# Kernel tuning notes

Measured on AMD Instinct MI355X. Metric: run time of the kernel, lower is better.

## Reference

```python
import jax, jax.numpy as jnp
import numpy as np

B, T, D = 16, 4096, 256


def setup_inputs() -> dict:
    key = jax.random.key(0)
    ks = jax.random.split(key, 10)
    s = 1.0 / np.sqrt(D)  # torch nn.Linear default init range
    inp = {
        "x": jax.random.normal(ks[0], (B, T, D), jnp.float32),
        "hidden": jax.random.normal(ks[1], (B, D), jnp.float32),
    }
    names = ["W0", "b0", "W1", "b1", "W2", "b2", "W3", "b3"]
    for i, n in enumerate(names):
        shape = (D, D) if n.startswith("W") else (D,)
        inp[n] = jax.random.uniform(ks[2 + i], shape, jnp.float32, -s, s)
    return inp


def _gln(x, W0, b0, W1, b1, W2, b2, W3, b3):
    # Two gated-linear blocks; the final Linear(hyper[-1], hidden_size) in the
    # original module is never applied by calc_gln (index == len-1 is skipped).
    h = (x @ W0.T + b0) * jax.nn.sigmoid(x @ W1.T + b1)
    return (h @ W2.T + b2) * jax.nn.sigmoid(h @ W3.T + b3)


def reference(x, hidden, W0, b0, W1, b1, W2, b2, W3, b3):
    b = _gln(x, W0, b0, W1, b1, W2, b2, W3, b3)  # [B, T, D]
    bt = jnp.swapaxes(b, 0, 1)  # [T, B, D] for time-major scan
    init = jax.nn.relu(bt[0] + jnp.roll(hidden, 1, -1))

    def step(prev, b_t):
        out = jax.nn.relu(b_t + jnp.roll(prev, 1, -1))
        return out, out

    last, ys = jax.lax.scan(step, init, bt[1:])
    outputs = jnp.concatenate([init[None], ys], axis=0)  # [T, B, D]
    outputs = jnp.swapaxes(outputs, 0, 1)  # [B, T, D]; squeeze(2) is a no-op for D>1
    return outputs, last
```

## Files before the change

kernel.cpp:

```cpp
#include <hip/hip_runtime.h>
#include <hip/hip_bf16.h>
#include <cstdint>
#include <cstddef>

typedef __bf16 bf16x8 __attribute__((ext_vector_type(8)));
typedef float  f32x4  __attribute__((ext_vector_type(4)));

static constexpr int B  = 16;
static constexpr int T  = 4096;
static constexpr int D  = 256;
static constexpr int M  = B * T;
static constexpr int SEGS = 64;
static constexpr int SEGL = T / SEGS;

__global__ void cvt_w(const float* __restrict__ W0, const float* __restrict__ W1,
                      const float* __restrict__ W2, const float* __restrict__ W3,
                      __bf16* __restrict__ wp) {
    int i = blockIdx.x * blockDim.x + threadIdx.x;
    int s    = i >> 14;
    int r    = i & 16383;
    int ks   = r >> 11;
    int fg   = (r >> 6) & 31;
    int lane = r & 63;
    int kg = lane >> 4, rl = lane & 15;
    int w = fg >> 2, f = fg & 3;
    int q = f >> 1, gate = f & 1;
    int rc = w * 32 + 2 * rl + q;
    const float* src = (s == 0) ? (gate ? W1 : W0) : (gate ? W3 : W2);
    const float* p = src + (size_t)rc * 256 + ks * 32 + kg * 8;
    bf16x8 o;
#pragma unroll
    for (int j = 0; j < 8; ++j) o[j] = (__bf16)p[j];
    *reinterpret_cast<bf16x8*>(wp + (size_t)s * 131072 +
                               ((size_t)((ks * 32 + fg) * 64 + lane)) * 8) = o;
}

__launch_bounds__(512, 4)
__global__ void gln_fused(const float* __restrict__ x,
                          const __bf16* __restrict__ wp,
                          const float* __restrict__ b0, const float* __restrict__ b1,
                          const float* __restrict__ b2, const float* __restrict__ b3,
                          float* __restrict__ out) {
    __shared__ char xlds[32768];
    __shared__ char hlds[32768];

    const int tid  = threadIdx.x;
    const int lane = tid & 63;
    const int wid  = tid >> 6;
    const int rl   = lane & 15;
    const int kg   = lane >> 4;
    const int row0 = blockIdx.x * 64;

    {
        int r  = tid >> 3;
        int c0 = tid & 7;
        const float* xr = x + (size_t)(row0 + r) * 256;
        float4 xa[4][2];
#pragma unroll
        for (int ci = 0; ci < 4; ++ci) {
            const float4* p = reinterpret_cast<const float4*>(xr + (c0 + ci * 8) * 8);
            xa[ci][0] = p[0];
            xa[ci][1] = p[1];
        }
#pragma unroll
        for (int ci = 0; ci < 4; ++ci) {
            int ck = c0 + ci * 8;
            bf16x8 o = { (__bf16)xa[ci][0].x, (__bf16)xa[ci][0].y,
                         (__bf16)xa[ci][0].z, (__bf16)xa[ci][0].w,
                         (__bf16)xa[ci][1].x, (__bf16)xa[ci][1].y,
                         (__bf16)xa[ci][1].z, (__bf16)xa[ci][1].w };
            *reinterpret_cast<bf16x8*>(&xlds[r * 512 + ((ck ^ (r & 7)) * 16)]) = o;
        }
    }
    __syncthreads();

    f32x4 acc[4][4];

    auto run_stage = [&](const char* alds, const __bf16* wps) {
#pragma unroll
        for (int m = 0; m < 4; ++m)
#pragma unroll
            for (int f = 0; f < 4; ++f) acc[m][f] = (f32x4){0.f, 0.f, 0.f, 0.f};
#pragma unroll 2
        for (int ks = 0; ks < 8; ++ks) {
            bf16x8 bR[4], aR[4];
#pragma unroll
            for (int f = 0; f < 4; ++f)
                bR[f] = *reinterpret_cast<const bf16x8*>(
                    wps + ((size_t)((ks * 32 + (wid * 4 + f)) * 64 + lane)) * 8);
#pragma unroll
            for (int m = 0; m < 4; ++m) {
                int row = m * 16 + rl;
                int ck  = (ks * 4 + kg) ^ (rl & 7);
                aR[m] = *reinterpret_cast<const bf16x8*>(&alds[row * 512 + ck * 16]);
            }
#pragma unroll
            for (int m = 0; m < 4; ++m)
#pragma unroll
                for (int f = 0; f < 4; ++f)
                    acc[m][f] = __builtin_amdgcn_mfma_f32_16x16x32_bf16(
                        aR[m], bR[f], acc[m][f], 0, 0, 0);
        }
    };

    run_stage(xlds, wp);
    {
        int rc0 = wid * 32 + 2 * rl;
        float2 bb0 = *reinterpret_cast<const float2*>(b0 + rc0);
        float2 bb1 = *reinterpret_cast<const float2*>(b1 + rc0);
        int colb = rc0 * 2;
        int ckb  = colb >> 4;
        int off  = colb & 15;
#pragma unroll
        for (int m = 0; m < 4; ++m)
#pragma unroll
            for (int j = 0; j < 4; ++j) {
                int row = m * 16 + kg * 4 + j;
                float he = (acc[m][0][j] + bb0.x) *
                           (1.0f / (1.0f + __expf(-(acc[m][1][j] + bb1.x))));
                float ho = (acc[m][2][j] + bb0.y) *
                           (1.0f / (1.0f + __expf(-(acc[m][3][j] + bb1.y))));
                unsigned short ue = __builtin_bit_cast(unsigned short, (__bf16)he);
                unsigned short uo = __builtin_bit_cast(unsigned short, (__bf16)ho);
                unsigned int u = ((unsigned int)uo << 16) | (unsigned int)ue;
                *reinterpret_cast<unsigned int*>(
                    &hlds[row * 512 + ((ckb ^ (row & 7)) * 16) + off]) = u;
            }
    }
    __syncthreads();

    run_stage(hlds, wp + 131072);
    {
        int rc0 = wid * 32 + 2 * rl;
        float2 bb2 = *reinterpret_cast<const float2*>(b2 + rc0);
        float2 bb3 = *reinterpret_cast<const float2*>(b3 + rc0);
#pragma unroll
        for (int m = 0; m < 4; ++m)
#pragma unroll
            for (int j = 0; j < 4; ++j) {
                int row = m * 16 + kg * 4 + j;
                float he = (acc[m][0][j] + bb2.x) *
                           (1.0f / (1.0f + __expf(-(acc[m][1][j] + bb3.x))));
                float ho = (acc[m][2][j] + bb2.y) *
                           (1.0f / (1.0f + __expf(-(acc[m][3][j] + bb3.y))));
                float2 o; o.x = he; o.y = ho;
                *reinterpret_cast<float2*>(out + (size_t)(row0 + row) * 256 + rc0) = o;
            }
    }
}

__global__ void scan_seg(const float* __restrict__ bmat, float2* __restrict__ seg_am) {
    int tid   = blockIdx.x * blockDim.x + threadIdx.x;
    int c     = tid & 255;
    int rest  = tid >> 8;
    int batch = rest & 15;
    int seg   = rest >> 4;
    const float* base = bmat + (size_t)batch * T * D;
    float A = 0.f, Mx = -1e30f;
    int t0 = seg * SEGL;
#pragma unroll 8
    for (int i = 0; i < SEGL; ++i) {
        int t = t0 + i;
        float v = base[(size_t)t * 256 + ((c + t) & 255)];
        A += v;
        Mx = fmaxf(Mx + v, 0.f);
    }
    float2 o; o.x = A; o.y = Mx;
    seg_am[(size_t)(batch * SEGS + seg) * 256 + c] = o;
}

__global__ void scan_bound(const float2* __restrict__ seg_am,
                           const float* __restrict__ hidden,
                           float* __restrict__ seg_state) {
    int tid   = blockIdx.x * blockDim.x + threadIdx.x;
    int c     = tid & 255;
    int batch = tid >> 8;
    float s = hidden[batch * 256 + ((c + 255) & 255)];
    for (int seg = 0; seg < SEGS; ++seg) {
        seg_state[(size_t)(batch * SEGS + seg) * 256 + c] = s;
        float2 am = seg_am[(size_t)(batch * SEGS + seg) * 256 + c];
        s = fmaxf(s + am.x, am.y);
    }
}

__global__ void scan_apply(float* __restrict__ bio,
                           const float* __restrict__ seg_state,
                           float* __restrict__ last) {
    int tid   = blockIdx.x * blockDim.x + threadIdx.x;
    int c     = tid & 255;
    int rest  = tid >> 8;
    int batch = rest & 15;
    int seg   = rest >> 4;
    float s = seg_state[(size_t)(batch * SEGS + seg) * 256 + c];
    float* base = bio + (size_t)batch * T * D;
    int t0 = seg * SEGL;
#pragma unroll 8
    for (int i = 0; i < SEGL; ++i) {
        int t = t0 + i;
        size_t idx = (size_t)t * 256 + ((c + t) & 255);
        float v = base[idx];
        s = fmaxf(s + v, 0.f);
        base[idx] = s;
    }
    if (seg == SEGS - 1) last[batch * 256 + ((c + 255) & 255)] = s;
}

extern "C" void kernel_launch(void* const* d_in, const int* in_sizes, int n_in,
                              void* d_out, int out_size, void* d_ws, size_t ws_size,
                              hipStream_t stream) {
    const float* x      = (const float*)d_in[0];
    const float* hidden = (const float*)d_in[1];
    const float* W0 = (const float*)d_in[2];
    const float* b0 = (const float*)d_in[3];
    const float* W1 = (const float*)d_in[4];
    const float* b1 = (const float*)d_in[5];
    const float* W2 = (const float*)d_in[6];
    const float* b2 = (const float*)d_in[7];
    const float* W3 = (const float*)d_in[8];
    const float* b3 = (const float*)d_in[9];

    float* out  = (float*)d_out;
    float* last = out + (size_t)M * D;

    char* ws = (char*)d_ws;
    __bf16* wpb       = (__bf16*)ws;
    float2* seg_am    = (float2*)(ws + 524288);
    float*  seg_state = (float*)(ws + 524288 + 2097152);

    cvt_w<<<128, 256, 0, stream>>>(W0, W1, W2, W3, wpb);
    gln_fused<<<M / 64, 512, 0, stream>>>(x, wpb, b0, b1, b2, b3, out);

    scan_seg<<<(B * D * SEGS) / 256, 256, 0, stream>>>(out, seg_am);
    scan_bound<<<B * D / 256, 256, 0, stream>>>(seg_am, hidden, seg_state);
    scan_apply<<<(B * D * SEGS) / 256, 256, 0, stream>>>(out, seg_state, last);
}
```

Measured before the change: 97.29 us.

## Fuse segment scan reduction into GLN GEMM kernel epilogue via LDS tile

The per-segment scan reduction (sum and max-plus prefix) is moved into the GEMM kernel's epilogue. Each 64-row block stages its fp32 output tile in LDS (dynamic shared memory, 64KB) and 256 threads compute the segment summary from it. This drops the scan_seg kernel launch and its full re-read of the output from global memory. It also adds setprio around the MFMA loop, plus extra barriers and a serial 64-step loop on half the threads at the end of each block.

```diff
diff --git a/kernel.cpp b/kernel.cpp
--- a/kernel.cpp
+++ b/kernel.cpp
@@ -40,9 +40,12 @@
                           const __bf16* __restrict__ wp,
                           const float* __restrict__ b0, const float* __restrict__ b1,
                           const float* __restrict__ b2, const float* __restrict__ b3,
-                          float* __restrict__ out) {
-    __shared__ char xlds[32768];
-    __shared__ char hlds[32768];
+                          float* __restrict__ out,
+                          float2* __restrict__ seg_am) {
+    extern __shared__ char smem[];
+    char* xlds = smem;
+    char* hlds = smem + 32768;
+    float* ftile = reinterpret_cast<float*>(smem);
 
     const int tid  = threadIdx.x;
     const int lane = tid & 63;
@@ -94,12 +97,14 @@
                 int ck  = (ks * 4 + kg) ^ (rl & 7);
                 aR[m] = *reinterpret_cast<const bf16x8*>(&alds[row * 512 + ck * 16]);
             }
+            __builtin_amdgcn_s_setprio(1);
 #pragma unroll
             for (int m = 0; m < 4; ++m)
 #pragma unroll
                 for (int f = 0; f < 4; ++f)
                     acc[m][f] = __builtin_amdgcn_mfma_f32_16x16x32_bf16(
                         aR[m], bR[f], acc[m][f], 0, 0, 0);
+            __builtin_amdgcn_s_setprio(0);
         }
     };
 
@@ -130,6 +135,7 @@
     __syncthreads();
 
     run_stage(hlds, wp + 131072);
+    __syncthreads();
     {
         int rc0 = wid * 32 + 2 * rl;
         float2 bb2 = *reinterpret_cast<const float2*>(b2 + rc0);
@@ -145,28 +151,27 @@
                            (1.0f / (1.0f + __expf(-(acc[m][3][j] + bb3.y))));
                 float2 o; o.x = he; o.y = ho;
                 *reinterpret_cast<float2*>(out + (size_t)(row0 + row) * 256 + rc0) = o;
+                *reinterpret_cast<float2*>(ftile + row * 256 + rc0) = o;
             }
     }
-}
-
-__global__ void scan_seg(const float* __restrict__ bmat, float2* __restrict__ seg_am) {
-    int tid   = blockIdx.x * blockDim.x + threadIdx.x;
-    int c     = tid & 255;
-    int rest  = tid >> 8;
-    int batch = rest & 15;
-    int seg   = rest >> 4;
-    const float* base = bmat + (size_t)batch * T * D;
-    float A = 0.f, Mx = -1e30f;
-    int t0 = seg * SEGL;
+    __syncthreads();
+
+    if (tid < 256) {
+        int c     = tid;
+        int batch = row0 >> 12;
+        int t0    = row0 & 4095;
+        int seg   = t0 >> 6;
+        int cc    = (c + t0) & 255;
+        float A = 0.f, Mx = -1e30f;
 #pragma unroll 8
-    for (int i = 0; i < SEGL; ++i) {
-        int t = t0 + i;
-        float v = base[(size_t)t * 256 + ((c + t) & 255)];
-        A += v;
-        Mx = fmaxf(Mx + v, 0.f);
-    }
-    float2 o; o.x = A; o.y = Mx;
-    seg_am[(size_t)(batch * SEGS + seg) * 256 + c] = o;
+        for (int i = 0; i < SEGL; ++i) {
+            float v = ftile[i * 256 + ((cc + i) & 255)];
+            A += v;
+            Mx = fmaxf(Mx + v, 0.f);
+        }
+        float2 o; o.x = A; o.y = Mx;
+        seg_am[(size_t)(batch * SEGS + seg) * 256 + c] = o;
+    }
 }
 
 __global__ void scan_bound(const float2* __restrict__ seg_am,
@@ -227,10 +232,16 @@
     float2* seg_am    = (float2*)(ws + 524288);
     float*  seg_state = (float*)(ws + 524288 + 2097152);
 
+    static bool attr_done = false;
+    if (!attr_done) {
+        hipFuncSetAttribute(reinterpret_cast<const void*>(&gln_fused),
+                            hipFuncAttributeMaxDynamicSharedMemorySize, 65536);
+        attr_done = true;
+    }
+
     cvt_w<<<128, 256, 0, stream>>>(W0, W1, W2, W3, wpb);
-    gln_fused<<<M / 64, 512, 0, stream>>>(x, wpb, b0, b1, b2, b3, out);
-
-    scan_seg<<<(B * D * SEGS) / 256, 256, 0, stream>>>(out, seg_am);
+    gln_fused<<<M / 64, 512, 65536, stream>>>(x, wpb, b0, b1, b2, b3, out, seg_am);
+
     scan_bound<<<B * D / 256, 256, 0, stream>>>(seg_am, hidden, seg_state);
     scan_apply<<<(B * D * SEGS) / 256, 256, 0, stream>>>(out, seg_state, last);
 }
```

Result: faster. 93.63 us (-3.8%).

## Shrink GLN row tile to 32 with 16 waves and reuse one LDS buffer

Applied to the files above, without the earlier changes.

The fused GLN kernel now handles 32 rows per block with 1024 threads (16 waves split into 2 row groups × 8 column groups) instead of 64 rows with 8 waves. Each wave holds a single 16-row A fragment and 4 accumulators, not 4×4, which cuts register pressure. The x tile and the intermediate h tile share one 16 KB LDS buffer, with an added barrier before h overwrites it. In exchange, each block re-reads the full packed weights from global/L2 for half as many rows, doubling weight traffic per output row.

```diff
diff --git a/kernel.cpp b/kernel.cpp
--- a/kernel.cpp
+++ b/kernel.cpp
@@ -35,117 +35,99 @@
                                ((size_t)((ks * 32 + fg) * 64 + lane)) * 8) = o;
 }
 
-__launch_bounds__(512, 4)
+__launch_bounds__(1024, 8)
 __global__ void gln_fused(const float* __restrict__ x,
                           const __bf16* __restrict__ wp,
                           const float* __restrict__ b0, const float* __restrict__ b1,
                           const float* __restrict__ b2, const float* __restrict__ b3,
                           float* __restrict__ out) {
-    __shared__ char xlds[32768];
-    __shared__ char hlds[32768];
+    __shared__ char tile[16384];
 
     const int tid  = threadIdx.x;
     const int lane = tid & 63;
     const int wid  = tid >> 6;
     const int rl   = lane & 15;
     const int kg   = lane >> 4;
-    const int row0 = blockIdx.x * 64;
+    const int cw   = wid & 7;
+    const int rw   = wid >> 3;
+    const int row0 = blockIdx.x * 32;
+
+    const __bf16* wv0 = wp + ((size_t)(cw * 4) * 64 + lane) * 8;
+    const __bf16* wv1 = wv0 + 131072;
 
     {
-        int r  = tid >> 3;
-        int c0 = tid & 7;
-        const float* xr = x + (size_t)(row0 + r) * 256;
-        float4 xa[4][2];
-#pragma unroll
-        for (int ci = 0; ci < 4; ++ci) {
-            const float4* p = reinterpret_cast<const float4*>(xr + (c0 + ci * 8) * 8);
-            xa[ci][0] = p[0];
-            xa[ci][1] = p[1];
-        }
-#pragma unroll
-        for (int ci = 0; ci < 4; ++ci) {
-            int ck = c0 + ci * 8;
-            bf16x8 o = { (__bf16)xa[ci][0].x, (__bf16)xa[ci][0].y,
-                         (__bf16)xa[ci][0].z, (__bf16)xa[ci][0].w,
-                         (__bf16)xa[ci][1].x, (__bf16)xa[ci][1].y,
-                         (__bf16)xa[ci][1].z, (__bf16)xa[ci][1].w };
-            *reinterpret_cast<bf16x8*>(&xlds[r * 512 + ((ck ^ (r & 7)) * 16)]) = o;
-        }
+        int r  = tid >> 5;
+        int c0 = tid & 31;
+        const float4* p = reinterpret_cast<const float4*>(
+            x + (size_t)(row0 + r) * 256 + c0 * 8);
+        float4 v0 = p[0], v1 = p[1];
+        bf16x8 o = { (__bf16)v0.x, (__bf16)v0.y, (__bf16)v0.z, (__bf16)v0.w,
+                     (__bf16)v1.x, (__bf16)v1.y, (__bf16)v1.z, (__bf16)v1.w };
+        *reinterpret_cast<bf16x8*>(&tile[r * 512 + ((c0 ^ (r & 7)) * 16)]) = o;
     }
     __syncthreads();
 
-    f32x4 acc[4][4];
-
-    auto run_stage = [&](const char* alds, const __bf16* wps) {
-#pragma unroll
-        for (int m = 0; m < 4; ++m)
-#pragma unroll
-            for (int f = 0; f < 4; ++f) acc[m][f] = (f32x4){0.f, 0.f, 0.f, 0.f};
+    f32x4 acc[4];
+
+    auto run_stage = [&](const __bf16* wvb) {
+#pragma unroll
+        for (int f = 0; f < 4; ++f) acc[f] = (f32x4){0.f, 0.f, 0.f, 0.f};
+        const int arow = (rw * 16 + rl) * 512;
 #pragma unroll 2
         for (int ks = 0; ks < 8; ++ks) {
-            bf16x8 bR[4], aR[4];
+            bf16x8 bR[4];
 #pragma unroll
             for (int f = 0; f < 4; ++f)
-                bR[f] = *reinterpret_cast<const bf16x8*>(
-                    wps + ((size_t)((ks * 32 + (wid * 4 + f)) * 64 + lane)) * 8);
-#pragma unroll
-            for (int m = 0; m < 4; ++m) {
-                int row = m * 16 + rl;
-                int ck  = (ks * 4 + kg) ^ (rl & 7);
-                aR[m] = *reinterpret_cast<const bf16x8*>(&alds[row * 512 + ck * 16]);
-            }
-#pragma unroll
-            for (int m = 0; m < 4; ++m)
-#pragma unroll
-                for (int f = 0; f < 4; ++f)
-                    acc[m][f] = __builtin_amdgcn_mfma_f32_16x16x32_bf16(
-                        aR[m], bR[f], acc[m][f], 0, 0, 0);
+                bR[f] = *reinterpret_cast<const bf16x8*>(wvb + ks * 16384 + f * 512);
+            int ck = (ks * 4 + kg) ^ (rl & 7);
+            bf16x8 aR = *reinterpret_cast<const bf16x8*>(&tile[arow + ck * 16]);
+#pragma unroll
+            for (int f = 0; f < 4; ++f)
+                acc[f] = __builtin_amdgcn_mfma_f32_16x16x32_bf16(aR, bR[f], acc[f],
+                                                                 0, 0, 0);
         }
     };
 
-    run_stage(xlds, wp);
+    const int rc0 = cw * 32 + 2 * rl;
+
+    run_stage(wv0);
+    __syncthreads();
     {
-        int rc0 = wid * 32 + 2 * rl;
         float2 bb0 = *reinterpret_cast<const float2*>(b0 + rc0);
         float2 bb1 = *reinterpret_cast<const float2*>(b1 + rc0);
-        int colb = rc0 * 2;
-        int ckb  = colb >> 4;
-        int off  = colb & 15;
-#pragma unroll
-        for (int m = 0; m < 4; ++m)
-#pragma unroll
-            for (int j = 0; j < 4; ++j) {
-                int row = m * 16 + kg * 4 + j;
-                float he = (acc[m][0][j] + bb0.x) *
-                           (1.0f / (1.0f + __expf(-(acc[m][1][j] + bb1.x))));
-                float ho = (acc[m][2][j] + bb0.y) *
-                           (1.0f / (1.0f + __expf(-(acc[m][3][j] + bb1.y))));
-                unsigned short ue = __builtin_bit_cast(unsigned short, (__bf16)he);
-                unsigned short uo = __builtin_bit_cast(unsigned short, (__bf16)ho);
-                unsigned int u = ((unsigned int)uo << 16) | (unsigned int)ue;
-                *reinterpret_cast<unsigned int*>(
-                    &hlds[row * 512 + ((ckb ^ (row & 7)) * 16) + off]) = u;
-            }
+        int cb  = rc0 * 2;
+        int ck  = cb >> 4;
+        int off = cb & 15;
+#pragma unroll
+        for (int j = 0; j < 4; ++j) {
+            int row = rw * 16 + kg * 4 + j;
+            float he = (acc[0][j] + bb0.x) *
+                       (1.0f / (1.0f + __expf(-(acc[1][j] + bb1.x))));
+            float ho = (acc[2][j] + bb0.y) *
+                       (1.0f / (1.0f + __expf(-(acc[3][j] + bb1.y))));
+            unsigned short ue = __builtin_bit_cast(unsigned short, (__bf16)he);
+            unsigned short uo = __builtin_bit_cast(unsigned short, (__bf16)ho);
+            unsigned int u = ((unsigned int)uo << 16) | (unsigned int)ue;
+            *reinterpret_cast<unsigned int*>(
+                &tile[row * 512 + ((ck ^ (row & 7)) * 16) + off]) = u;
+        }
     }
     __syncthreads();
 
-    run_stage(hlds, wp + 131072);
+    run_stage(wv1);
     {
-        int rc0 = wid * 32 + 2 * rl;
         float2 bb2 = *reinterpret_cast<const float2*>(b2 + rc0);
         float2 bb3 = *reinterpret_cast<const float2*>(b3 + rc0);
 #pragma unroll
-        for (int m = 0; m < 4; ++m)
-#pragma unroll
-            for (int j = 0; j < 4; ++j) {
-                int row = m * 16 + kg * 4 + j;
-                float he = (acc[m][0][j] + bb2.x) *
-                           (1.0f / (1.0f + __expf(-(acc[m][1][j] + bb3.x))));
-                float ho = (acc[m][2][j] + bb2.y) *
-                           (1.0f / (1.0f + __expf(-(acc[m][3][j] + bb3.y))));
-                float2 o; o.x = he; o.y = ho;
-                *reinterpret_cast<float2*>(out + (size_t)(row0 + row) * 256 + rc0) = o;
-            }
+        for (int j = 0; j < 4; ++j) {
+            int row = rw * 16 + kg * 4 + j;
+            float he = (acc[0][j] + bb2.x) *
+                       (1.0f / (1.0f + __expf(-(acc[1][j] + bb3.x))));
+            float ho = (acc[2][j] + bb2.y) *
+                       (1.0f / (1.0f + __expf(-(acc[3][j] + bb3.y))));
+            float2 o; o.x = he; o.y = ho;
+            *reinterpret_cast<float2*>(out + (size_t)(row0 + row) * 256 + rc0) = o;
+        }
     }
 }
 
@@ -228,7 +210,7 @@
     float*  seg_state = (float*)(ws + 524288 + 2097152);
 
     cvt_w<<<128, 256, 0, stream>>>(W0, W1, W2, W3, wpb);
-    gln_fused<<<M / 64, 512, 0, stream>>>(x, wpb, b0, b1, b2, b3, out);
+    gln_fused<<<M / 32, 1024, 0, stream>>>(x, wpb, b0, b1, b2, b3, out);
 
     scan_seg<<<(B * D * SEGS) / 256, 256, 0, stream>>>(out, seg_am);
     scan_bound<<<B * D / 256, 256, 0, stream>>>(seg_am, hidden, seg_state);
```

Result: slower. 129.9 us (+33.5%).

## Double-buffer weight fragments, reuse one LDS tile, change swizzle pattern

Applied to the files above, without the earlier changes.

Weight fragments for the next k-step are now prefetched from global memory into registers while MFMAs run on the current step, and the k loop is fully unrolled. The x and h tiles share a single 32 KB LDS buffer, with an extra barrier before h overwrites x, which halves LDS use per block and may allow more resident blocks. The XOR swizzle now shifts the row bits by two, which changes the LDS bank-conflict pattern. The extra prefetch registers could raise register pressure against the launch bound.

```diff
diff --git a/kernel.cpp b/kernel.cpp
--- a/kernel.cpp
+++ b/kernel.cpp
@@ -41,8 +41,7 @@
                           const float* __restrict__ b0, const float* __restrict__ b1,
                           const float* __restrict__ b2, const float* __restrict__ b3,
                           float* __restrict__ out) {
-    __shared__ char xlds[32768];
-    __shared__ char hlds[32768];
+    __shared__ char tile[32768];
 
     const int tid  = threadIdx.x;
     const int lane = tid & 63;
@@ -51,6 +50,16 @@
     const int kg   = lane >> 4;
     const int row0 = blockIdx.x * 64;
 
+    const __bf16* wv0 = wp + ((size_t)(wid * 4) * 64 + lane) * 8;
+    const __bf16* wv1 = wv0 + 131072;
+
+    bf16x8 bbuf[2][4];
+    auto loadB = [&](int p, const __bf16* wvb, int ks) {
+#pragma unroll
+        for (int f = 0; f < 4; ++f)
+            bbuf[p][f] = *reinterpret_cast<const bf16x8*>(wvb + ks * 16384 + f * 512);
+    };
+
     {
         int r  = tid >> 3;
         int c0 = tid & 7;
@@ -65,52 +74,54 @@
 #pragma unroll
         for (int ci = 0; ci < 4; ++ci) {
             int ck = c0 + ci * 8;
+            int pc = ck ^ ((r & 7) << 2);
             bf16x8 o = { (__bf16)xa[ci][0].x, (__bf16)xa[ci][0].y,
                          (__bf16)xa[ci][0].z, (__bf16)xa[ci][0].w,
                          (__bf16)xa[ci][1].x, (__bf16)xa[ci][1].y,
                          (__bf16)xa[ci][1].z, (__bf16)xa[ci][1].w };
-            *reinterpret_cast<bf16x8*>(&xlds[r * 512 + ((ck ^ (r & 7)) * 16)]) = o;
+            *reinterpret_cast<bf16x8*>(&tile[r * 512 + pc * 16]) = o;
         }
     }
+    loadB(0, wv0, 0);
     __syncthreads();
 
     f32x4 acc[4][4];
 
-    auto run_stage = [&](const char* alds, const __bf16* wps) {
+    auto run_stage = [&](const __bf16* wvb) {
 #pragma unroll
         for (int m = 0; m < 4; ++m)
 #pragma unroll
             for (int f = 0; f < 4; ++f) acc[m][f] = (f32x4){0.f, 0.f, 0.f, 0.f};
-#pragma unroll 2
+#pragma unroll
         for (int ks = 0; ks < 8; ++ks) {
-            bf16x8 bR[4], aR[4];
-#pragma unroll
-            for (int f = 0; f < 4; ++f)
-                bR[f] = *reinterpret_cast<const bf16x8*>(
-                    wps + ((size_t)((ks * 32 + (wid * 4 + f)) * 64 + lane)) * 8);
+            if (ks < 7) loadB((ks + 1) & 1, wvb, ks + 1);
+            bf16x8 aR[4];
 #pragma unroll
             for (int m = 0; m < 4; ++m) {
                 int row = m * 16 + rl;
-                int ck  = (ks * 4 + kg) ^ (rl & 7);
-                aR[m] = *reinterpret_cast<const bf16x8*>(&alds[row * 512 + ck * 16]);
+                int pc  = (ks * 4 + kg) ^ ((row & 7) << 2);
+                aR[m] = *reinterpret_cast<const bf16x8*>(&tile[row * 512 + pc * 16]);
             }
 #pragma unroll
             for (int m = 0; m < 4; ++m)
 #pragma unroll
                 for (int f = 0; f < 4; ++f)
                     acc[m][f] = __builtin_amdgcn_mfma_f32_16x16x32_bf16(
-                        aR[m], bR[f], acc[m][f], 0, 0, 0);
+                        aR[m], bbuf[ks & 1][f], acc[m][f], 0, 0, 0);
         }
     };
 
-    run_stage(xlds, wp);
+    const int rc0 = wid * 32 + 2 * rl;
+
+    run_stage(wv0);
+    loadB(0, wv1, 0);
+    __syncthreads();
     {
-        int rc0 = wid * 32 + 2 * rl;
         float2 bb0 = *reinterpret_cast<const float2*>(b0 + rc0);
         float2 bb1 = *reinterpret_cast<const float2*>(b1 + rc0);
-        int colb = rc0 * 2;
-        int ckb  = colb >> 4;
-        int off  = colb & 15;
+        int cb  = rc0 * 2;
+        int ck  = cb >> 4;
+        int off = cb & 15;
 #pragma unroll
         for (int m = 0; m < 4; ++m)
 #pragma unroll
@@ -123,15 +134,14 @@
                 unsigned short ue = __builtin_bit_cast(unsigned short, (__bf16)he);
                 unsigned short uo = __builtin_bit_cast(unsigned short, (__bf16)ho);
                 unsigned int u = ((unsigned int)uo << 16) | (unsigned int)ue;
-                *reinterpret_cast<unsigned int*>(
-                    &hlds[row * 512 + ((ckb ^ (row & 7)) * 16) + off]) = u;
+                int pc = ck ^ ((row & 7) << 2);
+                *reinterpret_cast<unsigned int*>(&tile[row * 512 + pc * 16 + off]) = u;
             }
     }
     __syncthreads();
 
-    run_stage(hlds, wp + 131072);
+    run_stage(wv1);
     {
-        int rc0 = wid * 32 + 2 * rl;
         float2 bb2 = *reinterpret_cast<const float2*>(b2 + rc0);
         float2 bb3 = *reinterpret_cast<const float2*>(b3 + rc0);
 #pragma unroll
```

New measurement: 95.76 us. Within noise of the previous version (-1.6%).
